# Kernel tuning notes

Hardware: AMD Instinct MI355X
Metric: run time of the kernel (lower is better)

The kernel has to match this reference:

```python
import jax, jax.numpy as jnp
import numpy as np
from jax import lax

C = 256
HEADS = 8
H2 = HEADS // 2          # heads per branch
HD = C // HEADS          # head dim = 32
SR = 4                   # spatial reduction ratio
WS = 7                   # window size (hard-coded in source)
SCALE = HD ** -0.5
EPS = 1e-5


def _window_partition(t, H, W, D):
    # t: [B, h, N, c] -> [B*h*nW, WS^3, c]
    B, h, N, c = t.shape
    t = t.reshape(B * h, H // WS, WS, W // WS, WS, D // WS, WS, c)
    t = t.transpose(0, 1, 3, 5, 2, 4, 6, 7)
    return t.reshape(-1, WS * WS * WS, c)


def _window_reverse(w, H, W, D, head):
    # w: [BH*nW, WS^3, c] -> [B, N, head*c] (heads interleaved into channels)
    nW = (H // WS) * (W // WS) * (D // WS)
    BH = w.shape[0] // nW
    x = w.reshape(BH, H // WS, W // WS, D // WS, WS, WS, WS, -1)
    x = x.transpose(0, 1, 4, 2, 5, 3, 6, 7).reshape(BH, H, W, D, -1)
    B = BH // head
    x = x.reshape(B, head, H, W, D, -1).transpose(0, 2, 3, 4, 1, 5)
    return x.reshape(B, H * W * D, -1)


def setup_inputs() -> dict:
    key = jax.random.key(0)
    ks = jax.random.split(key, 16)
    B, H, W, D = 1, 28, 28, 28
    N = H * W * D
    tn = lambda k, shp: jax.random.normal(k, shp, jnp.float32) * 0.02
    # conv fan-out inits (per source _init_weights)
    lepe_fan = 3 * 3 * C // C  # depthwise: groups=C
    sr_fan = SR * SR * C
    return {
        "x": jax.random.normal(ks[0], (B, N, C), jnp.float32),
        "H": H, "W": W, "D": D,
        "lepe_w": tn(ks[1], (C, C)),
        "lepe_b": jnp.zeros((C,), jnp.float32),
        "lepe_conv_w": jax.random.normal(ks[2], (C, 1, 3, 3, 3), jnp.float32) * np.sqrt(2.0 / lepe_fan),
        "lepe_conv_b": jnp.zeros((C,), jnp.float32),
        "sr_w": jax.random.normal(ks[3], (C, C, SR, SR, SR), jnp.float32) * np.sqrt(2.0 / sr_fan),
        "sr_b": jnp.zeros((C,), jnp.float32),
        "norm_g": jnp.ones((C,), jnp.float32),
        "norm_b": jnp.zeros((C,), jnp.float32),
        "q1_w": tn(ks[4], (C // 2, C)),
        "kv1_w": tn(ks[5], (C, C)),
        "q2_w": tn(ks[6], (C // 2, C)),
        "kv2_w": tn(ks[7], (C, C)),
        "proj_w": tn(ks[8], (C, C)),
        "proj_b": jnp.zeros((C,), jnp.float32),
    }


def _forward(x, lepe_w, lepe_b, lepe_conv_w, lepe_conv_b, sr_w, sr_b,
             norm_g, norm_b, q1_w, kv1_w, q2_w, kv2_w, proj_w, proj_b,
             H, W, D):
    B, N, _ = x.shape
    # --- LePE: linear -> depthwise Conv3d over (H,W,D) ---
    y = x @ lepe_w.T + lepe_b                              # [B,N,C]
    y = y.transpose(0, 2, 1).reshape(B, C, H, W, D)
    lepe = lax.conv_general_dilated(
        y, lepe_conv_w, window_strides=(1, 1, 1), padding='SAME',
        dimension_numbers=('NCDHW', 'OIDHW', 'NCDHW'), feature_group_count=C)
    lepe = (lepe + lepe_conv_b[None, :, None, None, None])
    lepe = lepe.reshape(B, C, N).transpose(0, 2, 1)        # [B,N,C]

    x_ = x.transpose(0, 2, 1).reshape(B, C, H, W, D)

    # --- Branch 1: spatially-reduced global attention (heads 0..3) ---
    q1 = (x @ q1_w.T).reshape(B, N, H2, HD).transpose(0, 2, 1, 3)   # [B,h2,N,hd]
    x1 = lax.conv_general_dilated(
        x_, sr_w, window_strides=(SR, SR, SR), padding='VALID',
        dimension_numbers=('NCDHW', 'OIDHW', 'NCDHW'))
    x1 = x1 + sr_b[None, :, None, None, None]
    x1 = x1.reshape(B, C, -1).transpose(0, 2, 1)                    # [B,Nr,C]
    mu = x1.mean(-1, keepdims=True)
    var = ((x1 - mu) ** 2).mean(-1, keepdims=True)
    x1 = (x1 - mu) * lax.rsqrt(var + EPS) * norm_g + norm_b
    x1 = jax.nn.gelu(x1, approximate=False)
    Nr = x1.shape[1]
    kv1 = (x1 @ kv1_w.T).reshape(B, Nr, 2, H2, HD).transpose(2, 0, 3, 1, 4)
    k1, v1 = kv1[0], kv1[1]                                         # [B,h2,Nr,hd]
    attn1 = jax.nn.softmax(jnp.einsum('bhnd,bhmd->bhnm', q1, k1) * SCALE, axis=-1)
    o1 = jnp.einsum('bhnm,bhmd->bhnd', attn1, v1)
    o1 = o1.transpose(0, 2, 1, 3).reshape(B, N, C // 2)

    # --- Branch 2: windowed local attention (heads 4..7) ---
    q2 = (x @ q2_w.T).reshape(B, N, H2, HD).transpose(0, 2, 1, 3)
    kv2 = (x @ kv2_w.T).reshape(B, N, 2, H2, HD).transpose(2, 0, 3, 1, 4)
    k2, v2 = kv2[0], kv2[1]                                         # [B,h2,N,hd]
    q2w = _window_partition(q2, H, W, D)
    k2w = _window_partition(k2, H, W, D)
    v2w = _window_partition(v2, H, W, D)
    attn2 = jax.nn.softmax(jnp.einsum('wnd,wmd->wnm', q2w, k2w) * SCALE, axis=-1)
    o2 = jnp.einsum('wnm,wmd->wnd', attn2, v2w)
    o2 = _window_reverse(o2, H, W, D, H2)                           # [B,N,C/2]

    out = jnp.concatenate([o1, o2], axis=-1)
    return (out + lepe) @ proj_w.T + proj_b


def reference(x, H, W, D, lepe_w, lepe_b, lepe_conv_w, lepe_conv_b,
              sr_w, sr_b, norm_g, norm_b, q1_w, kv1_w, q2_w, kv2_w,
              proj_w, proj_b):
    return _forward(x, lepe_w, lepe_b, lepe_conv_w, lepe_conv_b, sr_w, sr_b,
                    norm_g, norm_b, q1_w, kv1_w, q2_w, kv2_w, proj_w, proj_b,
                    int(H), int(W), int(D))
```

## Files before the change

kernel.cpp:

```cpp
#include <hip/hip_runtime.h>

#define N_TOK 21952
#define NR    343
#define ATT_SCALE 0.17677669529663687f

typedef unsigned short u16;
typedef short  v8s __attribute__((ext_vector_type(8)));
typedef float  v4f __attribute__((ext_vector_type(4)));

__device__ __forceinline__ float bf2f(unsigned u) {
    return __builtin_bit_cast(float, u << 16);
}
__device__ __forceinline__ u16 f2bf(float f) {
    unsigned u = __builtin_bit_cast(unsigned, f);
    u += 0x7fffu + ((u >> 16) & 1u);
    return (u16)(u >> 16);
}
__device__ __forceinline__ unsigned bfadd2(unsigned a, unsigned b) {
    float lo = bf2f(a & 0xffffu) + bf2f(b & 0xffffu);
    float hi = bf2f(a >> 16)     + bf2f(b >> 16);
    return (unsigned)f2bf(lo) | ((unsigned)f2bf(hi) << 16);
}

__global__ __launch_bounds__(256) void convert_x_kernel(
    const float* __restrict__ x, u16* __restrict__ xb)
{
    size_t i = ((size_t)blockIdx.x * 256 + threadIdx.x) * 8;
    float4 a0 = *(const float4*)(x + i);
    float4 a1 = *(const float4*)(x + i + 4);
    uint4 av;
    av.x = (unsigned)f2bf(a0.x) | ((unsigned)f2bf(a0.y) << 16);
    av.y = (unsigned)f2bf(a0.z) | ((unsigned)f2bf(a0.w) << 16);
    av.z = (unsigned)f2bf(a1.x) | ((unsigned)f2bf(a1.y) << 16);
    av.w = (unsigned)f2bf(a1.z) | ((unsigned)f2bf(a1.w) << 16);
    *(uint4*)(xb + i) = av;
}

#define WSEG0 16384
#define WSEG1 24576
#define WSEG2 32768
#define WSEG3 49152
#define WSEG4 65536
#define WSEG5 81920
#define WSEG6 82112

__global__ __launch_bounds__(256) void convert_w_kernel(
    const float* __restrict__ wl,  const float* __restrict__ wq1,
    const float* __restrict__ wq2, const float* __restrict__ wk2,
    const float* __restrict__ wk1, const float* __restrict__ wp,
    const float* __restrict__ lepe_b,
    u16* wb_comb, u16* wb_k1, u16* wb_p, float* bias_all)
{
    int gid = blockIdx.x * 256 + threadIdx.x;
    if (gid >= WSEG6) return;
    if (gid >= WSEG5) {
        int b = gid - WSEG5;
        float4 v;
        int i = b * 4;
        v.x = (i + 0 < 256) ? lepe_b[i + 0] : 0.f;
        v.y = (i + 1 < 256) ? lepe_b[i + 1] : 0.f;
        v.z = (i + 2 < 256) ? lepe_b[i + 2] : 0.f;
        v.w = (i + 3 < 256) ? lepe_b[i + 3] : 0.f;
        *(float4*)(bias_all + i) = v;
        return;
    }
    const float* s; u16* d; int l; float sc = 1.f;
    if      (gid < WSEG0) { s = wl;  d = wb_comb;           l = gid; }
    else if (gid < WSEG1) { s = wq1; d = wb_comb + 65536;   l = gid - WSEG0; sc = ATT_SCALE; }
    else if (gid < WSEG2) { s = wq2; d = wb_comb + 98304;   l = gid - WSEG1; sc = ATT_SCALE; }
    else if (gid < WSEG3) { s = wk2; d = wb_comb + 131072;  l = gid - WSEG2; }
    else if (gid < WSEG4) { s = wk1; d = wb_k1;             l = gid - WSEG3; }
    else                  { s = wp;  d = wb_p;              l = gid - WSEG4; }
    float4 v = *(const float4*)(s + (size_t)l * 4);
    *(ushort4*)(d + (size_t)l * 4) =
        make_ushort4(f2bf(v.x * sc), f2bf(v.y * sc), f2bf(v.z * sc), f2bf(v.w * sc));
}

__global__ __launch_bounds__(256) void convert_sr_kernel(
    const float* __restrict__ wsr, u16* __restrict__ wt)
{
    int u  = blockIdx.x * 256 + threadIdx.x;
    int co = u >> 8, ci = u & 255;
    const float* src = wsr + (size_t)co * 16384 + ci * 64;
#pragma unroll
    for (int t4 = 0; t4 < 16; t4++) {
        float4 v = *(const float4*)(src + t4 * 4);
        int t = t4 * 4;
        wt[(size_t)(t + 0) * 65536 + co * 256 + ci] = f2bf(v.x);
        wt[(size_t)(t + 1) * 65536 + co * 256 + ci] = f2bf(v.y);
        wt[(size_t)(t + 2) * 65536 + co * 256 + ci] = f2bf(v.z);
        wt[(size_t)(t + 3) * 65536 + co * 256 + ci] = f2bf(v.w);
    }
}

#define LDA 40

template<bool HAS2>
__global__ __launch_bounds__(256, 3) void gemm_pipe(
    const u16* __restrict__ A, const u16* __restrict__ A2,
    const u16* __restrict__ W, const float* __restrict__ bias,
    void* __restrict__ outp, int M, int ldout, int mode, int nwg, int NT)
{
    __shared__ u16 Asm[2][128 * LDA];
    __shared__ u16 Bsm[2][64 * LDA];
    const int tid = threadIdx.x;

    int bid = blockIdx.x;
    int q = nwg >> 3, r8 = nwg & 7;
    int xcd = bid & 7, idx = bid >> 3;
    int wgid = (xcd < r8 ? xcd * (q + 1) : r8 * (q + 1) + (xcd - r8) * q) + idx;
    const int m0 = (wgid / NT) * 128;
    const int n0 = (wgid % NT) * 64;

    const int wave = tid >> 6, lane = tid & 63;
    const int wm = (wave & 1) * 64, wn = (wave >> 1) * 32;
    const int fr = lane & 15, fq = lane >> 4;

    const int ar0 = tid >> 2;
    const int ar1 = ar0 + 64;
    const int seg = (tid & 3) * 8;
    const bool g0 = (m0 + ar0) < M;
    const bool g1 = (m0 + ar1) < M;
    const u16* pA0 = A + (size_t)(m0 + ar0) * 256 + seg;
    const u16* pA1 = A + (size_t)(m0 + ar1) * 256 + seg;
    const u16* pB  = W + (size_t)(n0 + ar0) * 256 + seg;
    const u16* pC0 = HAS2 ? A2 + (size_t)(m0 + ar0) * 256 + seg : nullptr;
    const u16* pC1 = HAS2 ? A2 + (size_t)(m0 + ar1) * 256 + seg : nullptr;

    uint4 rA0[2], rA1[2], rB[2], rC0[2], rC1[2];
    const uint4 Z = make_uint4(0, 0, 0, 0);

#define G_LOAD(s, ph) do { int kk = (ph) * 32;                               \
        rA0[s] = g0 ? *(const uint4*)(pA0 + kk) : Z;                         \
        rA1[s] = g1 ? *(const uint4*)(pA1 + kk) : Z;                         \
        rB[s]  = *(const uint4*)(pB + kk);                                   \
        if (HAS2) {                                                          \
            rC0[s] = g0 ? *(const uint4*)(pC0 + kk) : Z;                     \
            rC1[s] = g1 ? *(const uint4*)(pC1 + kk) : Z;                     \
        } } while (0)

#define L_WRITE(s, buf) do { uint4 a0 = rA0[s], a1 = rA1[s];                 \
        if (HAS2) {                                                          \
            a0.x = bfadd2(a0.x, rC0[s].x); a0.y = bfadd2(a0.y, rC0[s].y);    \
            a0.z = bfadd2(a0.z, rC0[s].z); a0.w = bfadd2(a0.w, rC0[s].w);    \
            a1.x = bfadd2(a1.x, rC1[s].x); a1.y = bfadd2(a1.y, rC1[s].y);    \
            a1.z = bfadd2(a1.z, rC1[s].z); a1.w = bfadd2(a1.w, rC1[s].w);    \
        }                                                                    \
        *(uint4*)(Asm[buf] + ar0 * LDA + seg) = a0;                          \
        *(uint4*)(Asm[buf] + ar1 * LDA + seg) = a1;                          \
        *(uint4*)(Bsm[buf] + ar0 * LDA + seg) = rB[s]; } while (0)

    v4f acc[4][2];
#pragma unroll
    for (int i = 0; i < 4; i++)
#pragma unroll
        for (int j = 0; j < 2; j++) acc[i][j] = (v4f){0.f, 0.f, 0.f, 0.f};

    G_LOAD(0, 0);
    G_LOAD(1, 1);
    L_WRITE(0, 0);
    __syncthreads();

#pragma unroll
    for (int ph = 0; ph < 8; ph++) {
        const int cur = ph & 1;
        if (ph + 2 < 8) G_LOAD(cur, ph + 2);
        {
            v8s af[4], bf[2];
#pragma unroll
            for (int i = 0; i < 4; i++)
                af[i] = *(const v8s*)(Asm[cur] + (wm + i * 16 + fr) * LDA + fq * 8);
#pragma unroll
            for (int j = 0; j < 2; j++)
                bf[j] = *(const v8s*)(Bsm[cur] + (wn + j * 16 + fr) * LDA + fq * 8);
#pragma unroll
            for (int i = 0; i < 4; i++)
#pragma unroll
                for (int j = 0; j < 2; j++)
                    acc[i][j] = __builtin_amdgcn_mfma_f32_16x16x32_bf16(
                        af[i], bf[j], acc[i][j], 0, 0, 0);
        }
        if (ph + 1 < 8) L_WRITE(cur ^ 1, cur ^ 1);
        __syncthreads();
    }
#undef G_LOAD
#undef L_WRITE

    float* outf = (float*)outp;
    u16*   outb = (u16*)outp;
#pragma unroll
    for (int i = 0; i < 4; i++) {
#pragma unroll
        for (int j = 0; j < 2; j++) {
            int col = n0 + wn + j * 16 + fr;
#pragma unroll
            for (int rr = 0; rr < 4; rr++) {
                int row = m0 + wm + i * 16 + fq * 4 + rr;
                if (row >= M) continue;
                float v = acc[i][j][rr];
                if (bias) v += bias[col];
                if (mode == 0) outb[(size_t)row * ldout + col] = f2bf(v);
                else           outf[(size_t)row * ldout + col] = v;
            }
        }
    }
}

__global__ __launch_bounds__(256) void sr_gemm(
    const u16* __restrict__ xb, const u16* __restrict__ Wt,
    float* __restrict__ partials)
{
    __shared__ u16 Asm[2][128 * LDA];
    __shared__ u16 Bsm[2][64 * LDA];
    const int tid = threadIdx.x;
    const int m0 = blockIdx.x * 128;
    const int n0 = blockIdx.y * 64;
    const int z  = blockIdx.z;
    const int wave = tid >> 6, lane = tid & 63;
    const int wm = (wave & 1) * 64, wn = (wave >> 1) * 32;
    const int fr = lane & 15, fq = lane >> 4;

    const int r0 = tid >> 2;
    const int r1 = r0 + 64;
    const int seg = (tid & 3) * 8;
    const int p0 = m0 + r0, p1 = m0 + r1;
    const int pz0 = p0 / 49, pr0 = p0 % 49, py0 = pr0 / 7, px0 = pr0 % 7;
    const int pz1 = p1 / 49, pr1 = p1 % 49, py1 = pr1 / 7, px1 = pr1 % 7;
    const int nb0 = pz0 * 4 * 784 + py0 * 4 * 28 + px0 * 4;
    const int nb1 = pz1 * 4 * 784 + py1 * 4 * 28 + px1 * 4;

    uint4 rv0, rv1, rbv;
    const uint4 Z = make_uint4(0, 0, 0, 0);

    auto G_LOAD = [&](int it) {
        int tap = z * 2 + (it >> 3);
        int ci0 = (it & 7) * 32;
        int kz = tap >> 4, ky = (tap >> 2) & 3, kx = tap & 3;
        int koff = kz * 784 + ky * 28 + kx;
        rv0 = (p0 < NR) ? *(const uint4*)(xb + (size_t)(nb0 + koff) * 256 + ci0 + seg) : Z;
        rv1 = (p1 < NR) ? *(const uint4*)(xb + (size_t)(nb1 + koff) * 256 + ci0 + seg) : Z;
        rbv = *(const uint4*)(Wt + (size_t)tap * 65536 + (size_t)(n0 + r0) * 256 + ci0 + seg);
    };
    auto L_WRITE = [&](int buf) {
        *(uint4*)(Asm[buf] + r0 * LDA + seg) = rv0;
        *(uint4*)(Asm[buf] + r1 * LDA + seg) = rv1;
        *(uint4*)(Bsm[buf] + r0 * LDA + seg) = rbv;
    };

    v4f acc[4][2];
#pragma unroll
    for (int i = 0; i < 4; i++)
#pragma unroll
        for (int j = 0; j < 2; j++) acc[i][j] = (v4f){0.f, 0.f, 0.f, 0.f};

    G_LOAD(0);
    L_WRITE(0);
    __syncthreads();

    int cur = 0;
    for (int it = 0; it < 16; it++) {
        if (it + 1 < 16) G_LOAD(it + 1);
        {
            v8s af[4], bfr[2];
#pragma unroll
            for (int i = 0; i < 4; i++)
                af[i] = *(const v8s*)(Asm[cur] + (wm + i * 16 + fr) * LDA + fq * 8);
#pragma unroll
            for (int j = 0; j < 2; j++)
                bfr[j] = *(const v8s*)(Bsm[cur] + (wn + j * 16 + fr) * LDA + fq * 8);
#pragma unroll
            for (int i = 0; i < 4; i++)
#pragma unroll
                for (int j = 0; j < 2; j++)
                    acc[i][j] = __builtin_amdgcn_mfma_f32_16x16x32_bf16(
                        af[i], bfr[j], acc[i][j], 0, 0, 0);
        }
        if (it + 1 < 16) L_WRITE(cur ^ 1);
        __syncthreads();
        cur ^= 1;
    }

    float* dst = partials + (size_t)z * (NR * 256);
#pragma unroll
    for (int i = 0; i < 4; i++) {
#pragma unroll
        for (int j = 0; j < 2; j++) {
            int col = n0 + wn + j * 16 + fr;
#pragma unroll
            for (int r = 0; r < 4; r++) {
                int row = m0 + wm + i * 16 + fq * 4 + r;
                if (row < NR) dst[(size_t)row * 256 + col] = acc[i][j][r];
            }
        }
    }
}

__global__ __launch_bounds__(256) void ln_gelu_kernel(
    const float* __restrict__ partials, const float* __restrict__ srb,
    const float* __restrict__ g, const float* __restrict__ b,
    u16* __restrict__ out)
{
    int row = blockIdx.x, c = threadIdx.x;
    float v = srb[c];
#pragma unroll
    for (int s = 0; s < 32; s++)
        v += partials[(size_t)s * (NR * 256) + row * 256 + c];
    float s1 = v, s2 = v * v;
#pragma unroll
    for (int off = 1; off < 64; off <<= 1) {
        s1 += __shfl_xor(s1, off);
        s2 += __shfl_xor(s2, off);
    }
    __shared__ float ws[4], ws2[4];
    int wave = c >> 6, lane = c & 63;
    if (lane == 0) { ws[wave] = s1; ws2[wave] = s2; }
    __syncthreads();
    float mean = (ws[0] + ws[1] + ws[2] + ws[3]) * (1.f / 256.f);
    float m2   = (ws2[0] + ws2[1] + ws2[2] + ws2[3]) * (1.f / 256.f);
    float var  = m2 - mean * mean;
    float xn = (v - mean) * rsqrtf(var + 1e-5f) * g[c] + b[c];
    out[row * 256 + c] = f2bf(0.5f * xn * (1.f + erff(xn * 0.70710678118654752f)));
}

__global__ __launch_bounds__(256) void dwconv_kernel(
    const u16* __restrict__ xall, const float* __restrict__ w,
    const float* __restrict__ bias, u16* __restrict__ out)
{
    __shared__ float sm[216 * 64];
    __shared__ float sw[64 * 27];
    const int tid = threadIdx.x;
    const int t  = blockIdx.x;
    const int g  = blockIdx.y;
    const int tz = t / 49, tr = t % 49, ty = tr / 7, tx = tr % 7;

    for (int u = tid; u < 64 * 27; u += 256) sw[u] = w[g * 64 * 27 + u];

    for (int u = tid; u < 216 * 8; u += 256) {
        int r = u >> 3, c8 = (u & 7) * 8;
        int vz = tz * 4 - 1 + r / 36;
        int rem = r % 36;
        int vy = ty * 4 - 1 + rem / 6;
        int vx = tx * 4 - 1 + rem % 6;
        float f[8];
        if ((unsigned)vz < 28u && (unsigned)vy < 28u && (unsigned)vx < 28u) {
            int n = vz * 784 + vy * 28 + vx;
            uint4 raw = *(const uint4*)(xall + (size_t)n * 768 + g * 64 + c8);
            f[0] = bf2f(raw.x & 0xffffu); f[1] = bf2f(raw.x >> 16);
            f[2] = bf2f(raw.y & 0xffffu); f[3] = bf2f(raw.y >> 16);
            f[4] = bf2f(raw.z & 0xffffu); f[5] = bf2f(raw.z >> 16);
            f[6] = bf2f(raw.w & 0xffffu); f[7] = bf2f(raw.w >> 16);
        } else {
#pragma unroll
            for (int i = 0; i < 8; i++) f[i] = 0.f;
        }
        float* dst = &sm[r * 64 + c8];
        *(float4*)dst       = make_float4(f[0], f[1], f[2], f[3]);
        *(float4*)(dst + 4) = make_float4(f[4], f[5], f[6], f[7]);
    }
    __syncthreads();

    const int c  = tid & 63;
    const int ch = g * 64 + c;
    float wreg[27];
#pragma unroll
    for (int j = 0; j < 27; j++) wreg[j] = sw[c * 27 + j];
    const float bc = bias[ch];

    const int vbase = (tid >> 6) * 16;
    for (int v = vbase; v < vbase + 16; v++) {
        int vz = v >> 4, vy = (v >> 2) & 3, vx = v & 3;
        float a = bc;
#pragma unroll
        for (int dz = 0; dz < 3; dz++)
#pragma unroll
            for (int dy = 0; dy < 3; dy++)
#pragma unroll
                for (int dx = 0; dx < 3; dx++)
                    a = fmaf(sm[((vz + dz) * 36 + (vy + dy) * 6 + (vx + dx)) * 64 + c],
                             wreg[dz * 9 + dy * 3 + dx], a);
        int n = (tz * 4 + vz) * 784 + (ty * 4 + vy) * 28 + (tx * 4 + vx);
        out[(size_t)n * 256 + ch] = f2bf(a);
    }
}

#define KP  40
#define VTP 360
#define PP  40

__global__ __launch_bounds__(256) void attn_kernel(
    const u16* __restrict__ xall, const u16* __restrict__ kv1,
    u16* __restrict__ o)
{
    __shared__ u16 Ks[352 * KP];
    __shared__ u16 VTs[32 * VTP];
    __shared__ u16 Ps[4 * 16 * PP];
    const int tid = threadIdx.x;
    const int h  = blockIdx.y;
    const int bx = blockIdx.x;
    const bool br1 = bx < 63;
    const int qbase = bx * 352;
    const int wi = bx - 63;
    const int zb = (wi >> 4) & 3, yb = (wi >> 2) & 3, xw = wi & 3;
    const int mt0 = blockIdx.z * 11;
    const int wave = tid >> 6, lane = tid & 63;
    const int fr = lane & 15, fq = lane >> 4;

    for (int u = tid; u < 352 * 4; u += 256) {
        int r = u >> 2, seg = u & 3;
        uint4 kq = make_uint4(0, 0, 0, 0), vq = make_uint4(0, 0, 0, 0);
        if (r < NR) {
            const u16* kb;
            if (br1) {
                kb = kv1 + (size_t)r * 256 + h * 32;
            } else {
                int mz = r / 49, mr = r % 49, my = mr / 7, mx = mr % 7;
                int nk = (zb * 7 + mz) * 784 + (yb * 7 + my) * 28 + (xw * 7 + mx);
                kb = xall + (size_t)nk * 768 + 512 + h * 32;
            }
            kq = *(const uint4*)(kb + seg * 8);
            vq = *(const uint4*)(kb + 128 + seg * 8);
        }
        *(uint4*)(Ks + r * KP + seg * 8) = kq;
        int d0 = seg * 8;
        VTs[(d0 + 0) * VTP + r] = (u16)(vq.x & 0xffffu);
        VTs[(d0 + 1) * VTP + r] = (u16)(vq.x >> 16);
        VTs[(d0 + 2) * VTP + r] = (u16)(vq.y & 0xffffu);
        VTs[(d0 + 3) * VTP + r] = (u16)(vq.y >> 16);
        VTs[(d0 + 4) * VTP + r] = (u16)(vq.z & 0xffffu);
        VTs[(d0 + 5) * VTP + r] = (u16)(vq.z >> 16);
        VTs[(d0 + 6) * VTP + r] = (u16)(vq.w & 0xffffu);
        VTs[(d0 + 7) * VTP + r] = (u16)(vq.w >> 16);
    }
    __syncthreads();

    u16* Pw = Ps + wave * 16 * PP;
    for (int mt = mt0 + wave; mt < mt0 + 11; mt += 4) {
        v8s aq = {0, 0, 0, 0, 0, 0, 0, 0};
        if (br1) {
            int qrow = qbase + mt * 16 + fr;
            if (qrow < N_TOK)
                aq = *(const v8s*)(xall + (size_t)qrow * 768 + 256 + h * 32 + fq * 8);
        } else {
            int tw = mt * 16 + fr;
            if (tw < NR) {
                int wz = tw / 49, tr2 = tw % 49, wy = tr2 / 7, wx = tr2 % 7;
                int nq = (zb * 7 + wz) * 784 + (yb * 7 + wy) * 28 + (xw * 7 + wx);
                aq = *(const v8s*)(xall + (size_t)nq * 768 + 384 + h * 32 + fq * 8);
            }
        }

        v4f s[22];
#pragma unroll
        for (int t = 0; t < 22; t++) {
            v8s bk = *(const v8s*)(Ks + (t * 16 + fr) * KP + fq * 8);
            s[t] = __builtin_amdgcn_mfma_f32_16x16x32_bf16(
                aq, bk, (v4f){0.f, 0.f, 0.f, 0.f}, 0, 0, 0);
        }
        if (fr >= 7) {
#pragma unroll
            for (int r = 0; r < 4; r++) s[21][r] = -1e30f;
        }

        float inv_l[4];
#pragma unroll
        for (int r = 0; r < 4; r++) {
            float m = s[0][r];
#pragma unroll
            for (int t = 1; t < 22; t++) m = fmaxf(m, s[t][r]);
#pragma unroll
            for (int off = 1; off < 16; off <<= 1) m = fmaxf(m, __shfl_xor(m, off));
            float l = 0.f;
#pragma unroll
            for (int t = 0; t < 22; t++) {
                v4f sv = s[t];
                float p = __expf(sv[r] - m);
                sv[r] = p; s[t] = sv;
                l += p;
            }
#pragma unroll
            for (int off = 1; off < 16; off <<= 1) l += __shfl_xor(l, off);
            inv_l[r] = 1.f / l;
        }

        v4f o0 = {0.f, 0.f, 0.f, 0.f}, o1 = {0.f, 0.f, 0.f, 0.f};
#pragma unroll
        for (int kt = 0; kt < 11; kt++) {
#pragma unroll
            for (int tt = 0; tt < 2; tt++) {
                int t = kt * 2 + tt;
#pragma unroll
                for (int r = 0; r < 4; r++)
                    Pw[(fq * 4 + r) * PP + tt * 16 + fr] = f2bf(s[t][r]);
            }
            __asm__ volatile("s_waitcnt lgkmcnt(0)" ::: "memory");
            v8s ap  = *(const v8s*)(Pw + fr * PP + fq * 8);
            v8s bv0 = *(const v8s*)(VTs + fr * VTP + kt * 32 + fq * 8);
            v8s bv1 = *(const v8s*)(VTs + (16 + fr) * VTP + kt * 32 + fq * 8);
            o0 = __builtin_amdgcn_mfma_f32_16x16x32_bf16(ap, bv0, o0, 0, 0, 0);
            o1 = __builtin_amdgcn_mfma_f32_16x16x32_bf16(ap, bv1, o1, 0, 0, 0);
        }

#pragma unroll
        for (int r = 0; r < 4; r++) {
            int rloc = mt * 16 + fq * 4 + r;
            u16* op = nullptr;
            if (br1) {
                int n = qbase + rloc;
                if (n < N_TOK) op = o + (size_t)n * 256 + h * 32;
            } else {
                if (rloc < NR) {
                    int wz = rloc / 49, tr2 = rloc % 49, wy = tr2 / 7, wx = tr2 % 7;
                    int nq = (zb * 7 + wz) * 784 + (yb * 7 + wy) * 28 + (xw * 7 + wx);
                    op = o + (size_t)nq * 256 + 128 + h * 32;
                }
            }
            if (op) {
                op[fr]      = f2bf(o0[r] * inv_l[r]);
                op[16 + fr] = f2bf(o1[r] * inv_l[r]);
            }
        }
    }
}

extern "C" void kernel_launch(void* const* d_in, const int* in_sizes, int n_in,
                              void* d_out, int out_size, void* d_ws, size_t ws_size,
                              hipStream_t stream)
{
    const float* x       = (const float*)d_in[0];
    const float* lepe_w  = (const float*)d_in[4];
    const float* lepe_b  = (const float*)d_in[5];
    const float* lconv_w = (const float*)d_in[6];
    const float* lconv_b = (const float*)d_in[7];
    const float* sr_w    = (const float*)d_in[8];
    const float* sr_b    = (const float*)d_in[9];
    const float* norm_g  = (const float*)d_in[10];
    const float* norm_b  = (const float*)d_in[11];
    const float* q1_w    = (const float*)d_in[12];
    const float* kv1_w   = (const float*)d_in[13];
    const float* q2_w    = (const float*)d_in[14];
    const float* kv2_w   = (const float*)d_in[15];
    const float* proj_w  = (const float*)d_in[16];
    const float* proj_b  = (const float*)d_in[17];
    float* out = (float*)d_out;

    const size_t NC = (size_t)N_TOK * 256;

    float* partials = (float*)d_ws;
    float* bias_all = partials + 32 * (NR * 256);
    u16* xb     = (u16*)(bias_all + 768);
    u16* xall   = xb + NC;
    u16* lepeb  = xall + (size_t)N_TOK * 768;
    u16* colb   = lepeb + NC;
    u16* x1b    = colb + NC;
    u16* kv1b   = x1b + NR * 256;
    u16* wb_comb = kv1b + NR * 256;
    u16* wb_k1  = wb_comb + 196608;
    u16* wb_p   = wb_k1 + 65536;
    u16* wsr_t  = wb_p + 65536;
    size_t need = (size_t)(32 * NR * 256 + 768) * 4 +
                  (NC + (size_t)N_TOK * 768 + 3 * NC + 2 * (size_t)NR * 256 +
                   196608 + 2 * 65536 + 4194304) * 2;
    if (ws_size < need) return;

    convert_w_kernel<<<dim3(321), 256, 0, stream>>>(
        lepe_w, q1_w, q2_w, kv2_w, kv1_w, proj_w, lepe_b,
        wb_comb, wb_k1, wb_p, bias_all);
    convert_sr_kernel<<<dim3(256), 256, 0, stream>>>(sr_w, wsr_t);
    convert_x_kernel<<<dim3(2744), 256, 0, stream>>>(x, xb);
    gemm_pipe<false><<<dim3(172 * 12), 256, 0, stream>>>(
        xb, nullptr, wb_comb, bias_all, xall, N_TOK, 768, 0, 172 * 12, 12);
    dwconv_kernel<<<dim3(343, 4), 256, 0, stream>>>(xall, lconv_w, lconv_b, lepeb);
    sr_gemm<<<dim3(3, 4, 32), 256, 0, stream>>>(xb, wsr_t, partials);
    ln_gelu_kernel<<<dim3(NR), 256, 0, stream>>>(partials, sr_b, norm_g, norm_b, x1b);
    gemm_pipe<false><<<dim3(3 * 4), 256, 0, stream>>>(
        x1b, nullptr, wb_k1, nullptr, kv1b, NR, 256, 0, 3 * 4, 4);
    attn_kernel<<<dim3(127, 4, 2), 256, 0, stream>>>(xall, kv1b, colb);
    gemm_pipe<true><<<dim3(172 * 4), 256, 0, stream>>>(
        colb, lepeb, wb_p, proj_b, out, N_TOK, 256, 1, 172 * 4, 4);
}
```

Measured before the change: 288.6 us.

## Use direct global-to-LDS loads in GEMM and fuse lepe add into attention

Replaces the register-staged, double-buffered GEMM with a single-buffered kernel that loads A/B tiles straight into LDS via global_load_lds, clamping out-of-range rows instead of zero-filling. bf16 outputs are now staged through LDS for coalesced 16-byte stores. The lepe residual add moves from the projection GEMM's A-load into the attention epilogue, so the projection GEMM reads one input instead of two. Dropping double buffering may expose load latency, which higher occupancy (launch bounds 4) is meant to hide.

```diff
diff --git a/kernel.cpp b/kernel.cpp
--- a/kernel.cpp
+++ b/kernel.cpp
@@ -16,10 +16,12 @@
     u += 0x7fffu + ((u >> 16) & 1u);
     return (u16)(u >> 16);
 }
-__device__ __forceinline__ unsigned bfadd2(unsigned a, unsigned b) {
-    float lo = bf2f(a & 0xffffu) + bf2f(b & 0xffffu);
-    float hi = bf2f(a >> 16)     + bf2f(b >> 16);
-    return (unsigned)f2bf(lo) | ((unsigned)f2bf(hi) << 16);
+
+__device__ __forceinline__ void gload_lds16(const u16* g, u16* l) {
+    __builtin_amdgcn_global_load_lds(
+        (const __attribute__((address_space(1))) unsigned*)g,
+        (__attribute__((address_space(3))) unsigned*)(unsigned)(uintptr_t)l,
+        16, 0, 0);
 }
 
 __global__ __launch_bounds__(256) void convert_x_kernel(
@@ -93,16 +95,14 @@
     }
 }
 
-#define LDA 40
-
-template<bool HAS2>
-__global__ __launch_bounds__(256, 3) void gemm_pipe(
-    const u16* __restrict__ A, const u16* __restrict__ A2,
-    const u16* __restrict__ W, const float* __restrict__ bias,
-    void* __restrict__ outp, int M, int ldout, int mode, int nwg, int NT)
-{
-    __shared__ u16 Asm[2][128 * LDA];
-    __shared__ u16 Bsm[2][64 * LDA];
+__global__ __launch_bounds__(256, 4) void gemm_lds(
+    const u16* __restrict__ A, const u16* __restrict__ W,
+    const float* __restrict__ bias, void* __restrict__ outp,
+    int M, int ldout, int mode, int nwg, int NT)
+{
+    __shared__ u16 smbuf[128 * 64];
+    u16* Asm = smbuf;
+    u16* Bsm = smbuf + 128 * 32;
     const int tid = threadIdx.x;
 
     int bid = blockIdx.x;
@@ -116,39 +116,15 @@
     const int wm = (wave & 1) * 64, wn = (wave >> 1) * 32;
     const int fr = lane & 15, fq = lane >> 4;
 
-    const int ar0 = tid >> 2;
-    const int ar1 = ar0 + 64;
-    const int seg = (tid & 3) * 8;
-    const bool g0 = (m0 + ar0) < M;
-    const bool g1 = (m0 + ar1) < M;
-    const u16* pA0 = A + (size_t)(m0 + ar0) * 256 + seg;
-    const u16* pA1 = A + (size_t)(m0 + ar1) * 256 + seg;
-    const u16* pB  = W + (size_t)(n0 + ar0) * 256 + seg;
-    const u16* pC0 = HAS2 ? A2 + (size_t)(m0 + ar0) * 256 + seg : nullptr;
-    const u16* pC1 = HAS2 ? A2 + (size_t)(m0 + ar1) * 256 + seg : nullptr;
-
-    uint4 rA0[2], rA1[2], rB[2], rC0[2], rC1[2];
-    const uint4 Z = make_uint4(0, 0, 0, 0);
-
-#define G_LOAD(s, ph) do { int kk = (ph) * 32;                               \
-        rA0[s] = g0 ? *(const uint4*)(pA0 + kk) : Z;                         \
-        rA1[s] = g1 ? *(const uint4*)(pA1 + kk) : Z;                         \
-        rB[s]  = *(const uint4*)(pB + kk);                                   \
-        if (HAS2) {                                                          \
-            rC0[s] = g0 ? *(const uint4*)(pC0 + kk) : Z;                     \
-            rC1[s] = g1 ? *(const uint4*)(pC1 + kk) : Z;                     \
-        } } while (0)
-
-#define L_WRITE(s, buf) do { uint4 a0 = rA0[s], a1 = rA1[s];                 \
-        if (HAS2) {                                                          \
-            a0.x = bfadd2(a0.x, rC0[s].x); a0.y = bfadd2(a0.y, rC0[s].y);    \
-            a0.z = bfadd2(a0.z, rC0[s].z); a0.w = bfadd2(a0.w, rC0[s].w);    \
-            a1.x = bfadd2(a1.x, rC1[s].x); a1.y = bfadd2(a1.y, rC1[s].y);    \
-            a1.z = bfadd2(a1.z, rC1[s].z); a1.w = bfadd2(a1.w, rC1[s].w);    \
-        }                                                                    \
-        *(uint4*)(Asm[buf] + ar0 * LDA + seg) = a0;                          \
-        *(uint4*)(Asm[buf] + ar1 * LDA + seg) = a1;                          \
-        *(uint4*)(Bsm[buf] + ar0 * LDA + seg) = rB[s]; } while (0)
+    const int l4 = lane >> 2, lc = (lane & 3) * 8;
+    int ra0 = m0 + wave * 32 + l4;  if (ra0 >= M) ra0 = M - 1;
+    int ra1 = ra0 + 16;             if (ra1 >= M) ra1 = M - 1;
+    const u16* gA0 = A + (size_t)ra0 * 256 + lc;
+    const u16* gA1 = A + (size_t)ra1 * 256 + lc;
+    const u16* gB  = W + (size_t)(n0 + wave * 16 + l4) * 256 + lc;
+    u16* ldsA0 = Asm + (wave * 32) * 32;
+    u16* ldsA1 = Asm + (wave * 32 + 16) * 32;
+    u16* ldsB  = Bsm + (wave * 16) * 32;
 
     v4f acc[4][2];
 #pragma unroll
@@ -156,55 +132,72 @@
 #pragma unroll
         for (int j = 0; j < 2; j++) acc[i][j] = (v4f){0.f, 0.f, 0.f, 0.f};
 
-    G_LOAD(0, 0);
-    G_LOAD(1, 1);
-    L_WRITE(0, 0);
-    __syncthreads();
-
-#pragma unroll
-    for (int ph = 0; ph < 8; ph++) {
-        const int cur = ph & 1;
-        if (ph + 2 < 8) G_LOAD(cur, ph + 2);
-        {
-            v8s af[4], bf[2];
-#pragma unroll
-            for (int i = 0; i < 4; i++)
-                af[i] = *(const v8s*)(Asm[cur] + (wm + i * 16 + fr) * LDA + fq * 8);
+    for (int kk = 0; kk < 256; kk += 32) {
+        gload_lds16(gA0 + kk, ldsA0);
+        gload_lds16(gA1 + kk, ldsA1);
+        gload_lds16(gB  + kk, ldsB);
+        __syncthreads();
+
+        v8s af[4], bf[2];
+#pragma unroll
+        for (int i = 0; i < 4; i++)
+            af[i] = *(const v8s*)(Asm + (wm + i * 16 + fr) * 32 + fq * 8);
+#pragma unroll
+        for (int j = 0; j < 2; j++)
+            bf[j] = *(const v8s*)(Bsm + (wn + j * 16 + fr) * 32 + fq * 8);
+#pragma unroll
+        for (int i = 0; i < 4; i++)
 #pragma unroll
             for (int j = 0; j < 2; j++)
-                bf[j] = *(const v8s*)(Bsm[cur] + (wn + j * 16 + fr) * LDA + fq * 8);
-#pragma unroll
-            for (int i = 0; i < 4; i++)
-#pragma unroll
-                for (int j = 0; j < 2; j++)
-                    acc[i][j] = __builtin_amdgcn_mfma_f32_16x16x32_bf16(
-                        af[i], bf[j], acc[i][j], 0, 0, 0);
-        }
-        if (ph + 1 < 8) L_WRITE(cur ^ 1, cur ^ 1);
+                acc[i][j] = __builtin_amdgcn_mfma_f32_16x16x32_bf16(
+                    af[i], bf[j], acc[i][j], 0, 0, 0);
         __syncthreads();
     }
-#undef G_LOAD
-#undef L_WRITE
-
-    float* outf = (float*)outp;
-    u16*   outb = (u16*)outp;
-#pragma unroll
-    for (int i = 0; i < 4; i++) {
-#pragma unroll
-        for (int j = 0; j < 2; j++) {
-            int col = n0 + wn + j * 16 + fr;
-#pragma unroll
-            for (int rr = 0; rr < 4; rr++) {
-                int row = m0 + wm + i * 16 + fq * 4 + rr;
-                if (row >= M) continue;
-                float v = acc[i][j][rr];
-                if (bias) v += bias[col];
-                if (mode == 0) outb[(size_t)row * ldout + col] = f2bf(v);
-                else           outf[(size_t)row * ldout + col] = v;
-            }
-        }
-    }
-}
+
+    if (mode == 0) {
+#pragma unroll
+        for (int i = 0; i < 4; i++)
+#pragma unroll
+            for (int j = 0; j < 2; j++) {
+                int col = wn + j * 16 + fr;
+#pragma unroll
+                for (int rr = 0; rr < 4; rr++) {
+                    int row = wm + i * 16 + fq * 4 + rr;
+                    float v = acc[i][j][rr];
+                    if (bias) v += bias[n0 + col];
+                    smbuf[row * 64 + col] = f2bf(v);
+                }
+            }
+        __syncthreads();
+#pragma unroll
+        for (int i = 0; i < 4; i++) {
+            int u = tid + i * 256;
+            int row = u >> 3, seg = (u & 7) * 8;
+            if (m0 + row < M) {
+                uint4 a = *(const uint4*)(smbuf + row * 64 + seg);
+                *(uint4*)((u16*)outp + (size_t)(m0 + row) * ldout + n0 + seg) = a;
+            }
+        }
+    } else {
+        float* outf = (float*)outp;
+#pragma unroll
+        for (int i = 0; i < 4; i++)
+#pragma unroll
+            for (int j = 0; j < 2; j++) {
+                int col = n0 + wn + j * 16 + fr;
+#pragma unroll
+                for (int rr = 0; rr < 4; rr++) {
+                    int row = m0 + wm + i * 16 + fq * 4 + rr;
+                    if (row >= M) continue;
+                    float v = acc[i][j][rr];
+                    if (bias) v += bias[col];
+                    outf[(size_t)row * ldout + col] = v;
+                }
+            }
+    }
+}
+
+#define LDA 40
 
 __global__ __launch_bounds__(256) void sr_gemm(
     const u16* __restrict__ xb, const u16* __restrict__ Wt,
@@ -389,7 +382,7 @@
 
 __global__ __launch_bounds__(256) void attn_kernel(
     const u16* __restrict__ xall, const u16* __restrict__ kv1,
-    u16* __restrict__ o)
+    const u16* __restrict__ lepe, u16* __restrict__ o)
 {
     __shared__ u16 Ks[352 * KP];
     __shared__ u16 VTs[32 * VTP];
@@ -503,20 +496,22 @@
 #pragma unroll
         for (int r = 0; r < 4; r++) {
             int rloc = mt * 16 + fq * 4 + r;
-            u16* op = nullptr;
+            size_t noff = 0; bool ok = false;
             if (br1) {
                 int n = qbase + rloc;
-                if (n < N_TOK) op = o + (size_t)n * 256 + h * 32;
+                if (n < N_TOK) { noff = (size_t)n * 256 + h * 32; ok = true; }
             } else {
                 if (rloc < NR) {
                     int wz = rloc / 49, tr2 = rloc % 49, wy = tr2 / 7, wx = tr2 % 7;
                     int nq = (zb * 7 + wz) * 784 + (yb * 7 + wy) * 28 + (xw * 7 + wx);
-                    op = o + (size_t)nq * 256 + 128 + h * 32;
+                    noff = (size_t)nq * 256 + 128 + h * 32; ok = true;
                 }
             }
-            if (op) {
-                op[fr]      = f2bf(o0[r] * inv_l[r]);
-                op[16 + fr] = f2bf(o1[r] * inv_l[r]);
+            if (ok) {
+                const u16* lp = lepe + noff;
+                u16* op = o + noff;
+                op[fr]      = f2bf(o0[r] * inv_l[r] + bf2f(lp[fr]));
+                op[16 + fr] = f2bf(o1[r] * inv_l[r] + bf2f(lp[16 + fr]));
             }
         }
     }
@@ -567,14 +562,14 @@
         wb_comb, wb_k1, wb_p, bias_all);
     convert_sr_kernel<<<dim3(256), 256, 0, stream>>>(sr_w, wsr_t);
     convert_x_kernel<<<dim3(2744), 256, 0, stream>>>(x, xb);
-    gemm_pipe<false><<<dim3(172 * 12), 256, 0, stream>>>(
-        xb, nullptr, wb_comb, bias_all, xall, N_TOK, 768, 0, 172 * 12, 12);
+    gemm_lds<<<dim3(172 * 12), 256, 0, stream>>>(
+        xb, wb_comb, bias_all, xall, N_TOK, 768, 0, 172 * 12, 12);
     dwconv_kernel<<<dim3(343, 4), 256, 0, stream>>>(xall, lconv_w, lconv_b, lepeb);
     sr_gemm<<<dim3(3, 4, 32), 256, 0, stream>>>(xb, wsr_t, partials);
     ln_gelu_kernel<<<dim3(NR), 256, 0, stream>>>(partials, sr_b, norm_g, norm_b, x1b);
-    gemm_pipe<false><<<dim3(3 * 4), 256, 0, stream>>>(
-        x1b, nullptr, wb_k1, nullptr, kv1b, NR, 256, 0, 3 * 4, 4);
-    attn_kernel<<<dim3(127, 4, 2), 256, 0, stream>>>(xall, kv1b, colb);
-    gemm_pipe<true><<<dim3(172 * 4), 256, 0, stream>>>(
-        colb, lepeb, wb_p, proj_b, out, N_TOK, 256, 1, 172 * 4, 4);
-}
+    gemm_lds<<<dim3(3 * 4), 256, 0, stream>>>(
+        x1b, wb_k1, nullptr, kv1b, NR, 256, 0, 3 * 4, 4);
+    attn_kernel<<<dim3(127, 4, 2), 256, 0, stream>>>(xall, kv1b, lepeb, colb);
+    gemm_lds<<<dim3(172 * 4), 256, 0, stream>>>(
+        colb, wb_p, proj_b, out, N_TOK, 256, 1, 172 * 4, 4);
+}
```

Measured after the change: 262.1 us. 1.1x faster.
